# Kernel tuning notes

Measured on AMD Instinct MI355X. Metric: run time of the kernel, lower is better.

## Reference

```python
import jax, jax.numpy as jnp
import numpy as np

K = 2            # top-k experts
TEMPERATURE = 1.0
EPS = 1e-9


def setup_inputs() -> dict:
    key = jax.random.key(0)
    k1, k2 = jax.random.split(key)
    B, S, D = 4, 4096, 4096
    G, E = 4, 64
    x = jax.random.normal(k1, (B, S, D), dtype=jnp.float32)
    # stacked gate weights, one [E, D] Linear weight per gate head
    W = jax.random.normal(k2, (G, E, D), dtype=jnp.float32) * 0.02
    return {"x": x, "W": W}


def reference(x, W):
    # per-head logits over experts: [B, S, G, E]; jitter disabled (eval / jitter_noise=0)
    logits = jnp.einsum('bsd,ged->bsge', x, W) * (1.0 / TEMPERATURE)
    probs = jax.nn.softmax(logits, axis=-1)          # softmax per head
    probs_full = probs.mean(axis=2)                  # consensus over heads: [B, S, E]
    topk_vals, idx = jax.lax.top_k(probs_full, K)    # sorted descending, matches aten.topk
    den = jnp.sum(topk_vals, axis=-1, keepdims=True)
    scores = topk_vals / jnp.maximum(den, EPS)       # clamp_min(den, 1e-9)
    pf = jax.lax.stop_gradient(probs_full)           # aux stats under no_grad
    importance = pf.mean(axis=(0, 1))                # [E]
    load = (pf > 0.0).astype(pf.dtype).mean(axis=(0, 1))  # [E]
    return idx, scores, probs_full, importance, load
```

## Files before the change

kernel.cpp:

```cpp
#include <hip/hip_runtime.h>

typedef _Float16 f16x8 __attribute__((ext_vector_type(8)));
typedef float    f32x4 __attribute__((ext_vector_type(4)));

#define MROWS 16384
#define NCOLS 256
#define KDIM  4096
#define BM    128
#define BK    32
#define LDA   40

#define OUT_SCORES 32768
#define OUT_PF     65536
#define OUT_IMP    1114112
#define OUT_LOAD   1114176

__global__ __launch_bounds__(256) void wprep(const float* __restrict__ W,
                                             _Float16* __restrict__ wfHi,
                                             _Float16* __restrict__ wfLo) {
    int t   = blockIdx.x * 256 + threadIdx.x;
    int l   = t & 63;
    int NT  = (t >> 6) & 15;
    int ksg = t >> 10;
    int n   = NT * 16 + (l & 15);
    int k   = ksg * 32 + ((l >> 4) << 3);
    const float* src = W + ((size_t)n * KDIM + (size_t)k);
    f16x8 hi, lo;
#pragma unroll
    for (int j = 0; j < 8; ++j) {
        float x = src[j];
        _Float16 h = (_Float16)x;
        hi[j] = h;
        lo[j] = (_Float16)(x - (float)h);
    }
    *(f16x8*)(wfHi + (size_t)t * 8) = hi;
    *(f16x8*)(wfLo + (size_t)t * 8) = lo;
}

__global__ __launch_bounds__(256, 2) void gemm3(const float* __restrict__ X,
        const _Float16* __restrict__ wfHi, const _Float16* __restrict__ wfLo,
        float* __restrict__ lsplit, int kQ) {
    __shared__ _Float16 aHi[2][BM * LDA];
    __shared__ _Float16 aLo[2][BM * LDA];

    const int tid  = threadIdx.x;
    const int lane = tid & 63;
    const int w    = tid >> 6;
    const int mt   = blockIdx.x & 127;
    const int s    = blockIdx.x >> 7;
    const int m0   = mt * BM;
    const int k0   = s * kQ;
    const int iters = kQ / BK;

    f32x4 acc[8][4];
#pragma unroll
    for (int a = 0; a < 8; ++a)
#pragma unroll
        for (int b = 0; b < 4; ++b) acc[a][b] = (f32x4){0.f, 0.f, 0.f, 0.f};

    const int sr = tid >> 1;
    const int sh = tid & 1;
    const float* xrow = X + ((size_t)(m0 + sr) * KDIM + (size_t)k0 + sh * 16);
    const int woff = sr * LDA + sh * 16;

    const int roff = (lane & 15) * LDA + (lane >> 4) * 8;

    size_t bbase = (((size_t)(k0 >> 5) * 16 + (size_t)w * 4) * 64 + (size_t)lane) * 8;
    const _Float16* pBH = wfHi + bbase;
    const _Float16* pBL = wfLo + bbase;

    {
        f32x4 v[4];
#pragma unroll
        for (int q = 0; q < 4; ++q) v[q] = *(const f32x4*)(xrow + q * 4);
        f16x8 h0, h1, l0, l1;
#pragma unroll
        for (int j = 0; j < 8; ++j) {
            float a = v[j >> 2][j & 3];
            _Float16 ha = (_Float16)a;
            h0[j] = ha; l0[j] = (_Float16)(a - (float)ha);
            float b = v[2 + (j >> 2)][j & 3];
            _Float16 hb = (_Float16)b;
            h1[j] = hb; l1[j] = (_Float16)(b - (float)hb);
        }
        *(f16x8*)(&aHi[0][woff])     = h0;
        *(f16x8*)(&aHi[0][woff + 8]) = h1;
        *(f16x8*)(&aLo[0][woff])     = l0;
        *(f16x8*)(&aLo[0][woff + 8]) = l1;
    }
    __syncthreads();

    for (int i = 0; i < iters; ++i) {
        const int cur = i & 1;

        f32x4 nx[4];
        const bool more = (i + 1 < iters);
        if (more) {
            const float* xp = xrow + (size_t)(i + 1) * BK;
#pragma unroll
            for (int q = 0; q < 4; ++q) nx[q] = *(const f32x4*)(xp + q * 4);
        }

        f16x8 bH[4], bL[4];
#pragma unroll
        for (int ni = 0; ni < 4; ++ni) {
            bH[ni] = *(const f16x8*)(pBH + (size_t)ni * 512);
            bL[ni] = *(const f16x8*)(pBL + (size_t)ni * 512);
        }
        pBH += 16 * 512;
        pBL += 16 * 512;

#pragma unroll
        for (int mi = 0; mi < 8; ++mi) {
            f16x8 aH = *(const f16x8*)(&aHi[cur][roff + mi * 16 * LDA]);
            f16x8 aL = *(const f16x8*)(&aLo[cur][roff + mi * 16 * LDA]);
#pragma unroll
            for (int ni = 0; ni < 4; ++ni) {
                acc[mi][ni] = __builtin_amdgcn_mfma_f32_16x16x32_f16(aH, bH[ni], acc[mi][ni], 0, 0, 0);
                acc[mi][ni] = __builtin_amdgcn_mfma_f32_16x16x32_f16(aH, bL[ni], acc[mi][ni], 0, 0, 0);
                acc[mi][ni] = __builtin_amdgcn_mfma_f32_16x16x32_f16(aL, bH[ni], acc[mi][ni], 0, 0, 0);
            }
        }

        if (more) {
            const int nxt = cur ^ 1;
            f16x8 h0, h1, l0, l1;
#pragma unroll
            for (int j = 0; j < 8; ++j) {
                float a = nx[j >> 2][j & 3];
                _Float16 ha = (_Float16)a;
                h0[j] = ha; l0[j] = (_Float16)(a - (float)ha);
                float b = nx[2 + (j >> 2)][j & 3];
                _Float16 hb = (_Float16)b;
                h1[j] = hb; l1[j] = (_Float16)(b - (float)hb);
            }
            *(f16x8*)(&aHi[nxt][woff])     = h0;
            *(f16x8*)(&aHi[nxt][woff + 8]) = h1;
            *(f16x8*)(&aLo[nxt][woff])     = l0;
            *(f16x8*)(&aLo[nxt][woff + 8]) = l1;
        }
        __syncthreads();
    }

    float* outp = lsplit + (size_t)s * ((size_t)MROWS * NCOLS);
#pragma unroll
    for (int mi = 0; mi < 8; ++mi) {
#pragma unroll
        for (int ni = 0; ni < 4; ++ni) {
            int col   = w * 64 + ni * 16 + (lane & 15);
            int rbase = m0 + mi * 16 + ((lane >> 4) << 2);
#pragma unroll
            for (int r = 0; r < 4; ++r)
                outp[(size_t)(rbase + r) * NCOLS + col] = acc[mi][ni][r];
        }
    }
}

__global__ __launch_bounds__(256) void finalize(const float* __restrict__ lsplit,
                                                int nsplit, float* __restrict__ out) {
    __shared__ float sImp[64], sLoad[64];
    const int tid = threadIdx.x;
    if (tid < 64) { sImp[tid] = 0.f; sLoad[tid] = 0.f; }
    __syncthreads();

    const int i   = tid & 15;
    const int grp = tid >> 4;
    const int r   = blockIdx.x * 16 + grp;

    float v[16];
#pragma unroll
    for (int t = 0; t < 16; ++t) {
        size_t off = (size_t)r * 256 + (size_t)i + 16 * t;
        float a = lsplit[off];
        for (int s = 1; s < nsplit; ++s)
            a += lsplit[(size_t)s * ((size_t)MROWS * NCOLS) + off];
        v[t] = a;
    }

    float hm[4];
#pragma unroll
    for (int g = 0; g < 4; ++g) {
        float m = fmaxf(fmaxf(v[4*g], v[4*g+1]), fmaxf(v[4*g+2], v[4*g+3]));
#pragma unroll
        for (int msk = 1; msk < 16; msk <<= 1)
            m = fmaxf(m, __shfl_xor(m, msk));
        hm[g] = m;
    }
    float p[16], inv[4];
#pragma unroll
    for (int g = 0; g < 4; ++g) {
        float sa = 0.f;
#pragma unroll
        for (int q = 0; q < 4; ++q) { p[4*g+q] = __expf(v[4*g+q] - hm[g]); sa += p[4*g+q]; }
#pragma unroll
        for (int msk = 1; msk < 16; msk <<= 1)
            sa += __shfl_xor(sa, msk);
        inv[g] = 1.f / sa;
    }

    float pf[4];
#pragma unroll
    for (int et = 0; et < 4; ++et) {
        pf[et] = 0.25f * (p[et] * inv[0] + p[4+et] * inv[1] + p[8+et] * inv[2] + p[12+et] * inv[3]);
        out[OUT_PF + (size_t)r * 64 + i + 16 * et] = pf[et];
        atomicAdd(&sImp[i + 16 * et], pf[et]);
        atomicAdd(&sLoad[i + 16 * et], pf[et] > 0.f ? 1.f : 0.f);
    }

    float v1 = -3.4e38f, v2 = -3.4e38f; int e1 = 0, e2 = 0;
#pragma unroll
    for (int et = 0; et < 4; ++et) {
        int e = i + 16 * et; float val = pf[et];
        if (val > v1) { v2 = v1; e2 = e1; v1 = val; e1 = e; }
        else if (val > v2) { v2 = val; e2 = e; }
    }
#pragma unroll
    for (int msk = 1; msk < 16; msk <<= 1) {
        float o1 = __shfl_xor(v1, msk); int oe1 = __shfl_xor(e1, msk);
        float o2 = __shfl_xor(v2, msk); int oe2 = __shfl_xor(e2, msk);
        bool ob = (o1 > v1) || (o1 == v1 && oe1 < e1);
        if (ob) {
            bool vb = (v1 > o2) || (v1 == o2 && e1 < oe2);
            v2 = vb ? v1 : o2; e2 = vb ? e1 : oe2;
            v1 = o1; e1 = oe1;
        } else {
            bool nb = (o1 > v2) || (o1 == v2 && oe1 < e2);
            v2 = nb ? o1 : v2; e2 = nb ? oe1 : e2;
        }
    }
    if (i == 0) {
        float den = fmaxf(v1 + v2, 1e-9f);
        out[(size_t)r * 2]              = (float)e1;
        out[(size_t)r * 2 + 1]          = (float)e2;
        out[OUT_SCORES + (size_t)r * 2]     = v1 / den;
        out[OUT_SCORES + (size_t)r * 2 + 1] = v2 / den;
    }
    __syncthreads();
    if (tid < 64) {
        atomicAdd(out + OUT_IMP  + tid, sImp[tid]  * (1.0f / 16384.0f));
        atomicAdd(out + OUT_LOAD + tid, sLoad[tid] * (1.0f / 16384.0f));
    }
}

extern "C" void kernel_launch(void* const* d_in, const int* in_sizes, int n_in,
                              void* d_out, int out_size, void* d_ws, size_t ws_size,
                              hipStream_t stream) {
    const float* X = (const float*)d_in[0];
    const float* W = (const float*)d_in[1];
    float* out = (float*)d_out;
    char* ws = (char*)d_ws;

    _Float16* wfHi = (_Float16*)ws;
    _Float16* wfLo = (_Float16*)(ws + (2u << 20));
    float* lsplit  = (float*)(ws + (4u << 20));

    const size_t per = 16u << 20;
    int nsplit = (ws_size >= (4u << 20) + 4 * per) ? 4
               : (ws_size >= (4u << 20) + 2 * per) ? 2 : 1;

    hipMemsetAsync((void*)(out + OUT_IMP), 0, 128 * sizeof(float), stream);

    wprep<<<512, 256, 0, stream>>>(W, wfHi, wfLo);
    gemm3<<<128 * nsplit, 256, 0, stream>>>(X, wfHi, wfLo, lsplit, KDIM / nsplit);
    finalize<<<1024, 256, 0, stream>>>(lsplit, nsplit, out);
}
```

Baseline: 463.3 us.

## Halve GEMM row tile, swizzle LDS A layout, vectorize finalize per wave

The GEMM row tile shrinks from 128 to 64, which doubles the block count and raises the occupancy hint to 4 blocks per CU. The A tile in shared memory moves from a padded row-major layout to a fragment-contiguous one, so each lane reads its MFMA operand with one contiguous 16-byte load. Finalize now has each wave process 16 rows using float4 loads and stores and keeps the importance and load sums in registers before the shared atomics. The cost is that each block reuses the B fragments across fewer rows, so W-fragment traffic from global memory roughly doubles.

Measured after the change: 460.5 us. No clear change (-0.6%).

```diff
diff --git a/kernel.cpp b/kernel.cpp
--- a/kernel.cpp
+++ b/kernel.cpp
@@ -6,9 +6,8 @@
 #define MROWS 16384
 #define NCOLS 256
 #define KDIM  4096
-#define BM    128
+#define BM    64
 #define BK    32
-#define LDA   40
 
 #define OUT_SCORES 32768
 #define OUT_PF     65536
@@ -37,83 +36,76 @@
     *(f16x8*)(wfLo + (size_t)t * 8) = lo;
 }
 
-__global__ __launch_bounds__(256, 2) void gemm3(const float* __restrict__ X,
+__global__ __launch_bounds__(256, 4) void gemm3(const float* __restrict__ X,
         const _Float16* __restrict__ wfHi, const _Float16* __restrict__ wfLo,
         float* __restrict__ lsplit, int kQ) {
-    __shared__ _Float16 aHi[2][BM * LDA];
-    __shared__ _Float16 aLo[2][BM * LDA];
+    __shared__ _Float16 aHi[2][2048];
+    __shared__ _Float16 aLo[2][2048];
 
     const int tid  = threadIdx.x;
     const int lane = tid & 63;
     const int w    = tid >> 6;
-    const int mt   = blockIdx.x & 127;
-    const int s    = blockIdx.x >> 7;
+    const int mt   = blockIdx.x & 255;
+    const int s    = blockIdx.x >> 8;
     const int m0   = mt * BM;
     const int k0   = s * kQ;
     const int iters = kQ / BK;
 
-    f32x4 acc[8][4];
-#pragma unroll
-    for (int a = 0; a < 8; ++a)
+    f32x4 acc[4][4];
+#pragma unroll
+    for (int a = 0; a < 4; ++a)
 #pragma unroll
         for (int b = 0; b < 4; ++b) acc[a][b] = (f32x4){0.f, 0.f, 0.f, 0.f};
 
-    const int sr = tid >> 1;
-    const int sh = tid & 1;
-    const float* xrow = X + ((size_t)(m0 + sr) * KDIM + (size_t)k0 + sh * 16);
-    const int woff = sr * LDA + sh * 16;
-
-    const int roff = (lane & 15) * LDA + (lane >> 4) * 8;
-
-    size_t bbase = (((size_t)(k0 >> 5) * 16 + (size_t)w * 4) * 64 + (size_t)lane) * 8;
+    const int sr = tid >> 2;
+    const int c  = tid & 3;
+    const float* xrow = X + ((size_t)(m0 + sr) * KDIM + (size_t)k0 + c * 8);
+    const int wgran = (((sr >> 4) * 4 + c) * 16 + (sr & 15)) * 8;
+
+    size_t bbase = ((size_t)(k0 >> 5) * 1024 + (size_t)w * 256 + (size_t)lane) * 8;
     const _Float16* pBH = wfHi + bbase;
     const _Float16* pBL = wfLo + bbase;
 
     {
-        f32x4 v[4];
-#pragma unroll
-        for (int q = 0; q < 4; ++q) v[q] = *(const f32x4*)(xrow + q * 4);
-        f16x8 h0, h1, l0, l1;
-#pragma unroll
-        for (int j = 0; j < 8; ++j) {
-            float a = v[j >> 2][j & 3];
-            _Float16 ha = (_Float16)a;
-            h0[j] = ha; l0[j] = (_Float16)(a - (float)ha);
-            float b = v[2 + (j >> 2)][j & 3];
-            _Float16 hb = (_Float16)b;
-            h1[j] = hb; l1[j] = (_Float16)(b - (float)hb);
-        }
-        *(f16x8*)(&aHi[0][woff])     = h0;
-        *(f16x8*)(&aHi[0][woff + 8]) = h1;
-        *(f16x8*)(&aLo[0][woff])     = l0;
-        *(f16x8*)(&aLo[0][woff + 8]) = l1;
+        f32x4 v0 = *(const f32x4*)(xrow);
+        f32x4 v1 = *(const f32x4*)(xrow + 4);
+        f16x8 h, l;
+#pragma unroll
+        for (int j = 0; j < 4; ++j) {
+            _Float16 ha = (_Float16)v0[j];
+            h[j] = ha; l[j] = (_Float16)(v0[j] - (float)ha);
+            _Float16 hb = (_Float16)v1[j];
+            h[4 + j] = hb; l[4 + j] = (_Float16)(v1[j] - (float)hb);
+        }
+        *(f16x8*)(&aHi[0][wgran]) = h;
+        *(f16x8*)(&aLo[0][wgran]) = l;
     }
     __syncthreads();
 
     for (int i = 0; i < iters; ++i) {
         const int cur = i & 1;
 
-        f32x4 nx[4];
+        f16x8 bH[4], bL[4];
+#pragma unroll
+        for (int ni = 0; ni < 4; ++ni) {
+            bH[ni] = *(const f16x8*)(pBH + (size_t)ni * 512);
+            bL[ni] = *(const f16x8*)(pBL + (size_t)ni * 512);
+        }
+        pBH += 8192;
+        pBL += 8192;
+
+        f32x4 nx0, nx1;
         const bool more = (i + 1 < iters);
         if (more) {
             const float* xp = xrow + (size_t)(i + 1) * BK;
-#pragma unroll
-            for (int q = 0; q < 4; ++q) nx[q] = *(const f32x4*)(xp + q * 4);
-        }
-
-        f16x8 bH[4], bL[4];
-#pragma unroll
-        for (int ni = 0; ni < 4; ++ni) {
-            bH[ni] = *(const f16x8*)(pBH + (size_t)ni * 512);
-            bL[ni] = *(const f16x8*)(pBL + (size_t)ni * 512);
-        }
-        pBH += 16 * 512;
-        pBL += 16 * 512;
-
-#pragma unroll
-        for (int mi = 0; mi < 8; ++mi) {
-            f16x8 aH = *(const f16x8*)(&aHi[cur][roff + mi * 16 * LDA]);
-            f16x8 aL = *(const f16x8*)(&aLo[cur][roff + mi * 16 * LDA]);
+            nx0 = *(const f32x4*)(xp);
+            nx1 = *(const f32x4*)(xp + 4);
+        }
+
+#pragma unroll
+        for (int mi = 0; mi < 4; ++mi) {
+            f16x8 aH = *(const f16x8*)(&aHi[cur][(mi * 64 + lane) * 8]);
+            f16x8 aL = *(const f16x8*)(&aLo[cur][(mi * 64 + lane) * 8]);
 #pragma unroll
             for (int ni = 0; ni < 4; ++ni) {
                 acc[mi][ni] = __builtin_amdgcn_mfma_f32_16x16x32_f16(aH, bH[ni], acc[mi][ni], 0, 0, 0);
@@ -124,27 +116,23 @@
 
         if (more) {
             const int nxt = cur ^ 1;
-            f16x8 h0, h1, l0, l1;
-#pragma unroll
-            for (int j = 0; j < 8; ++j) {
-                float a = nx[j >> 2][j & 3];
-                _Float16 ha = (_Float16)a;
-                h0[j] = ha; l0[j] = (_Float16)(a - (float)ha);
-                float b = nx[2 + (j >> 2)][j & 3];
-                _Float16 hb = (_Float16)b;
-                h1[j] = hb; l1[j] = (_Float16)(b - (float)hb);
+            f16x8 h, l;
+#pragma unroll
+            for (int j = 0; j < 4; ++j) {
+                _Float16 ha = (_Float16)nx0[j];
+                h[j] = ha; l[j] = (_Float16)(nx0[j] - (float)ha);
+                _Float16 hb = (_Float16)nx1[j];
+                h[4 + j] = hb; l[4 + j] = (_Float16)(nx1[j] - (float)hb);
             }
-            *(f16x8*)(&aHi[nxt][woff])     = h0;
-            *(f16x8*)(&aHi[nxt][woff + 8]) = h1;
-            *(f16x8*)(&aLo[nxt][woff])     = l0;
-            *(f16x8*)(&aLo[nxt][woff + 8]) = l1;
+            *(f16x8*)(&aHi[nxt][wgran]) = h;
+            *(f16x8*)(&aLo[nxt][wgran]) = l;
         }
         __syncthreads();
     }
 
     float* outp = lsplit + (size_t)s * ((size_t)MROWS * NCOLS);
 #pragma unroll
-    for (int mi = 0; mi < 8; ++mi) {
+    for (int mi = 0; mi < 4; ++mi) {
 #pragma unroll
         for (int ni = 0; ni < 4; ++ni) {
             int col   = w * 64 + ni * 16 + (lane & 15);
@@ -159,81 +147,91 @@
 __global__ __launch_bounds__(256) void finalize(const float* __restrict__ lsplit,
                                                 int nsplit, float* __restrict__ out) {
     __shared__ float sImp[64], sLoad[64];
-    const int tid = threadIdx.x;
+    const int tid  = threadIdx.x;
+    const int lane = tid & 63;
+    const int wv   = tid >> 6;
     if (tid < 64) { sImp[tid] = 0.f; sLoad[tid] = 0.f; }
     __syncthreads();
 
-    const int i   = tid & 15;
-    const int grp = tid >> 4;
-    const int r   = blockIdx.x * 16 + grp;
-
-    float v[16];
-#pragma unroll
-    for (int t = 0; t < 16; ++t) {
-        size_t off = (size_t)r * 256 + (size_t)i + 16 * t;
-        float a = lsplit[off];
+    const size_t SZ = (size_t)MROWS * NCOLS;
+    const int r0 = blockIdx.x * 64 + wv * 16;
+
+    f32x4 impAcc = (f32x4){0.f, 0.f, 0.f, 0.f};
+    f32x4 ldAcc  = (f32x4){0.f, 0.f, 0.f, 0.f};
+
+    for (int rr = 0; rr < 16; ++rr) {
+        const int r = r0 + rr;
+        const float* base = lsplit + (size_t)r * NCOLS + lane * 4;
+        f32x4 a = *(const f32x4*)(base);
         for (int s = 1; s < nsplit; ++s)
-            a += lsplit[(size_t)s * ((size_t)MROWS * NCOLS) + off];
-        v[t] = a;
-    }
-
-    float hm[4];
-#pragma unroll
-    for (int g = 0; g < 4; ++g) {
-        float m = fmaxf(fmaxf(v[4*g], v[4*g+1]), fmaxf(v[4*g+2], v[4*g+3]));
+            a += *(const f32x4*)(base + (size_t)s * SZ);
+
+        float m = fmaxf(fmaxf(a[0], a[1]), fmaxf(a[2], a[3]));
 #pragma unroll
         for (int msk = 1; msk < 16; msk <<= 1)
             m = fmaxf(m, __shfl_xor(m, msk));
-        hm[g] = m;
-    }
-    float p[16], inv[4];
-#pragma unroll
-    for (int g = 0; g < 4; ++g) {
+        f32x4 p;
         float sa = 0.f;
 #pragma unroll
-        for (int q = 0; q < 4; ++q) { p[4*g+q] = __expf(v[4*g+q] - hm[g]); sa += p[4*g+q]; }
+        for (int j = 0; j < 4; ++j) { p[j] = __expf(a[j] - m); sa += p[j]; }
 #pragma unroll
         for (int msk = 1; msk < 16; msk <<= 1)
             sa += __shfl_xor(sa, msk);
-        inv[g] = 1.f / sa;
-    }
-
-    float pf[4];
-#pragma unroll
-    for (int et = 0; et < 4; ++et) {
-        pf[et] = 0.25f * (p[et] * inv[0] + p[4+et] * inv[1] + p[8+et] * inv[2] + p[12+et] * inv[3]);
-        out[OUT_PF + (size_t)r * 64 + i + 16 * et] = pf[et];
-        atomicAdd(&sImp[i + 16 * et], pf[et]);
-        atomicAdd(&sLoad[i + 16 * et], pf[et] > 0.f ? 1.f : 0.f);
-    }
-
-    float v1 = -3.4e38f, v2 = -3.4e38f; int e1 = 0, e2 = 0;
-#pragma unroll
-    for (int et = 0; et < 4; ++et) {
-        int e = i + 16 * et; float val = pf[et];
-        if (val > v1) { v2 = v1; e2 = e1; v1 = val; e1 = e; }
-        else if (val > v2) { v2 = val; e2 = e; }
-    }
-#pragma unroll
-    for (int msk = 1; msk < 16; msk <<= 1) {
-        float o1 = __shfl_xor(v1, msk); int oe1 = __shfl_xor(e1, msk);
-        float o2 = __shfl_xor(v2, msk); int oe2 = __shfl_xor(e2, msk);
-        bool ob = (o1 > v1) || (o1 == v1 && oe1 < e1);
-        if (ob) {
-            bool vb = (v1 > o2) || (v1 == o2 && e1 < oe2);
-            v2 = vb ? v1 : o2; e2 = vb ? e1 : oe2;
-            v1 = o1; e1 = oe1;
-        } else {
-            bool nb = (o1 > v2) || (o1 == v2 && oe1 < e2);
-            v2 = nb ? o1 : v2; e2 = nb ? oe1 : e2;
-        }
-    }
-    if (i == 0) {
-        float den = fmaxf(v1 + v2, 1e-9f);
-        out[(size_t)r * 2]              = (float)e1;
-        out[(size_t)r * 2 + 1]          = (float)e2;
-        out[OUT_SCORES + (size_t)r * 2]     = v1 / den;
-        out[OUT_SCORES + (size_t)r * 2 + 1] = v2 / den;
+        float inv = 1.f / sa;
+#pragma unroll
+        for (int j = 0; j < 4; ++j) p[j] *= inv;
+
+        f32x4 pf;
+#pragma unroll
+        for (int j = 0; j < 4; ++j) {
+            float t = p[j];
+            t += __shfl_xor(t, 16);
+            t += __shfl_xor(t, 32);
+            pf[j] = t * 0.25f;
+        }
+
+        if (lane < 16)
+            *(f32x4*)(out + OUT_PF + (size_t)r * 64 + lane * 4) = pf;
+        impAcc += pf;
+#pragma unroll
+        for (int j = 0; j < 4; ++j) ldAcc[j] += (pf[j] > 0.f) ? 1.f : 0.f;
+
+        float v1 = -3.4e38f, v2 = -3.4e38f; int e1 = 0, e2 = 0;
+#pragma unroll
+        for (int j = 0; j < 4; ++j) {
+            int e = 4 * (lane & 15) + j; float val = pf[j];
+            if (val > v1) { v2 = v1; e2 = e1; v1 = val; e1 = e; }
+            else if (val > v2) { v2 = val; e2 = e; }
+        }
+#pragma unroll
+        for (int msk = 1; msk < 16; msk <<= 1) {
+            float o1 = __shfl_xor(v1, msk); int oe1 = __shfl_xor(e1, msk);
+            float o2 = __shfl_xor(v2, msk); int oe2 = __shfl_xor(e2, msk);
+            bool ob = (o1 > v1) || (o1 == v1 && oe1 < e1);
+            if (ob) {
+                bool vb = (v1 > o2) || (v1 == o2 && e1 < oe2);
+                v2 = vb ? v1 : o2; e2 = vb ? e1 : oe2;
+                v1 = o1; e1 = oe1;
+            } else {
+                bool nb = (o1 > v2) || (o1 == v2 && oe1 < e2);
+                v2 = nb ? o1 : v2; e2 = nb ? oe1 : e2;
+            }
+        }
+        if (lane == 0) {
+            float den = fmaxf(v1 + v2, 1e-9f);
+            out[(size_t)r * 2]                  = (float)e1;
+            out[(size_t)r * 2 + 1]              = (float)e2;
+            out[OUT_SCORES + (size_t)r * 2]     = v1 / den;
+            out[OUT_SCORES + (size_t)r * 2 + 1] = v2 / den;
+        }
+    }
+
+    if (lane < 16) {
+#pragma unroll
+        for (int j = 0; j < 4; ++j) {
+            atomicAdd(&sImp[4 * lane + j],  impAcc[j]);
+            atomicAdd(&sLoad[4 * lane + j], ldAcc[j]);
+        }
     }
     __syncthreads();
     if (tid < 64) {
@@ -261,6 +259,6 @@
     hipMemsetAsync((void*)(out + OUT_IMP), 0, 128 * sizeof(float), stream);
 
     wprep<<<512, 256, 0, stream>>>(W, wfHi, wfLo);
-    gemm3<<<128 * nsplit, 256, 0, stream>>>(X, wfHi, wfLo, lsplit, KDIM / nsplit);
-    finalize<<<1024, 256, 0, stream>>>(lsplit, nsplit, out);
-}
+    gemm3<<<256 * nsplit, 256, 0, stream>>>(X, wfHi, wfLo, lsplit, KDIM / nsplit);
+    finalize<<<256, 256, 0, stream>>>(lsplit, nsplit, out);
+}
```
